# Performance work log

Measured on AMD Instinct MI355X. Metric: run time of the kernel, lower is better.

The kernel has to match this reference:

```python
import jax, jax.numpy as jnp
import numpy as np

N = 2048   # nodes in the tree
K = 2      # max children (heap-ordered binary tree)
IN = 1024  # in_dim
M = 1024   # mem_dim
L = 1024   # rows of the fixed attention matrix


def setup_inputs() -> dict:
    key = jax.random.key(0)
    ks = jax.random.split(key, 12)
    s_in = 1.0 / np.sqrt(IN)
    s_m = 1.0 / np.sqrt(M)
    inputs = jax.random.normal(ks[0], (N, IN), jnp.float32)
    hiddn_state_mat = jax.random.normal(ks[1], (L, M), jnp.float32)
    # heap-ordered binary tree: children of i are 2i+1, 2i+2; -1 = no child.
    ch = np.full((N, K), -1, dtype=np.int64)
    for k in range(K):
        c = 2 * np.arange(N) + 1 + k
        ch[:, k] = np.where(c < N, c, -1)
    children = jnp.asarray(ch)
    u = lambda k, shape, s: jax.random.uniform(k, shape, jnp.float32, -s, s)
    params = dict(
        ioux_w=u(ks[2], (3 * M, IN), s_in), ioux_b=u(ks[3], (3 * M,), s_in),
        iouh_w=u(ks[4], (3 * M, M), s_m),  iouh_b=u(ks[5], (3 * M,), s_m),
        fx_w=u(ks[6], (M, IN), s_in),      fx_b=u(ks[7], (M,), s_in),
        fh_w=u(ks[8], (M, M), s_m),        fh_b=u(ks[9], (M,), s_m),
        Wa=-0.05 + 0.05 * jax.random.normal(ks[10], (1, M), jnp.float32),
        attnh_w=u(ks[11], (M, 2 * M), s_m),
        attnh_b=jnp.zeros((M,), jnp.float32),
    )
    return dict(inputs=inputs, hiddn_state_mat=hiddn_state_mat, children=children, **params)


def reference(inputs, hiddn_state_mat, children, ioux_w, ioux_b, iouh_w, iouh_b,
              fx_w, fx_b, fh_w, fh_b, Wa, attnh_w, attnh_b):
    mask = (children >= 0)
    safe = jnp.where(mask, children, 0)
    # split attnh into the part acting on h (first M cols) and on hiddn_state_mat
    W1 = attnh_w[:, :M]  # [M, M]
    W2 = attnh_w[:, M:]  # [M, M]
    HW2 = hiddn_state_mat @ W2.T  # [L, M], constant across nodes
    x_iou = inputs @ ioux_w.T + ioux_b  # [N, 3M]
    x_f = inputs @ fx_w.T + fx_b        # [N, M]

    def step(carry, t):
        C, Hs = carry  # [N, M] each
        m = mask[t].astype(inputs.dtype)[:, None]        # [K, 1]
        c_ch = C[safe[t]] * m                            # [K, M] (zeros for pads == torch leaf zeros)
        h_ch = Hs[safe[t]] * m                           # [K, M]
        h_sum = h_ch.sum(0)                              # [M]
        iou = x_iou[t] + h_sum @ iouh_w.T + iouh_b       # [3M]
        i, o, u = jnp.split(iou, 3)
        i, o, u = jax.nn.sigmoid(i), jax.nn.sigmoid(o), jnp.tanh(u)
        f = jax.nn.sigmoid(h_ch @ fh_w.T + fh_b + x_f[t])  # [K, M]
        c = i * u + (f * c_ch).sum(0)                    # [M]
        h = o * jnp.tanh(c)                              # [M]
        # attention over the fixed hidden-state matrix
        a = jnp.tanh(h @ W1.T + HW2 + attnh_b)           # [L, M]
        p = jax.nn.softmax(a @ Wa[0])                    # [L]
        # sum(p[:,None]*h_tiled, 0) == sum(p)*h since rows are identical
        h = ((1.0 - p)[:, None] * hiddn_state_mat).sum(0) + jnp.sum(p) * h
        return (C.at[t].set(c), Hs.at[t].set(h)), None

    C0 = jnp.zeros((N, M), inputs.dtype)
    Hs0 = jnp.zeros((N, M), inputs.dtype)
    order = jnp.arange(N - 1, -1, -1)  # leaves first, root (node 0) last
    (C, Hs), _ = jax.lax.scan(step, (C0, Hs0), order)
    return C[0:1], Hs[0:1], Hs  # (root c, root h, all hidden states)
```

## Files before the change

kernel.cpp:

```cpp
#include <hip/hip_runtime.h>
#include <hip/hip_bf16.h>

#define MD 1024
#define LD 1024
#define ND 2048
#define JZ 4096

typedef __bf16 bf16x8 __attribute__((ext_vector_type(8)));
typedef __bf16 bf16x4 __attribute__((ext_vector_type(4)));
typedef float  f32x4  __attribute__((ext_vector_type(4)));

__device__ __forceinline__ float fsig(float x)  { return 1.0f / (1.0f + __expf(-x)); }
__device__ __forceinline__ float ftanh_(float x){ float e = __expf(2.0f * x); return 1.0f - 2.0f / (e + 1.0f); }

__device__ __forceinline__ bf16x8 bzero8() {
    bf16x8 z;
    #pragma unroll
    for (int q = 0; q < 8; q++) z[q] = (__bf16)0.f;
    return z;
}

__global__ void cvt_rows_k(const float* __restrict__ src, int ld,
                           __bf16* __restrict__ dst, int K)
{
    int j = blockIdx.y;
    int k = blockIdx.x * 256 + threadIdx.x;
    dst[(size_t)j * K + k] = (__bf16)src[(size_t)j * ld + k];
}

__global__ void concat_bias_k(const float* __restrict__ a, const float* __restrict__ b,
                              float* __restrict__ dst)
{
    int i = blockIdx.x * 256 + threadIdx.x;
    dst[i] = (i < 3 * MD) ? a[i] : b[i - 3 * MD];
}

__global__ __launch_bounds__(256) void gemm_mfma(
    const __bf16* __restrict__ Ab, const float* __restrict__ Af, int amode, int lda,
    const __bf16* __restrict__ Wh,
    const float* __restrict__ bias,
    const float* __restrict__ X, int ldx, const float* __restrict__ add1,
    float* __restrict__ C, float* __restrict__ C2, __bf16* __restrict__ C3, int ldc,
    int I, int K, float scale, int epi)
{
    __shared__ __align__(16) __bf16 Ash[4][128][8];
    __shared__ __align__(16) __bf16 Bsh[4][128][8];
    const int tid = threadIdx.x;
    const int j0 = blockIdx.x * 128, i0 = blockIdx.y * 128;
    const int lane = tid & 63, wv = tid >> 6;
    const int wm = wv >> 1, wn = wv & 1;
    const int g = lane >> 4, fr = lane & 15;

    f32x4 acc[4][4];
    #pragma unroll
    for (int m = 0; m < 4; m++)
        #pragma unroll
        for (int n = 0; n < 4; n++)
            acc[m][n] = (f32x4){0.f, 0.f, 0.f, 0.f};

    const int srow = tid >> 1;
    const int kh   = (tid & 1) * 16;
    const int g0   = kh >> 3;
    const int arow = i0 + srow;
    const bool rowok = arow < I;
    const __bf16* Wrow = Wh + (size_t)(j0 + srow) * K + kh;
    const __bf16* Abr = Ab + (size_t)arow * lda + kh;
    const float*  Afr = Af + (size_t)arow * lda + kh;

    for (int kt = 0; kt < K; kt += 32) {
        bf16x8 a0, a1;
        if (amode == 0) {
            if (rowok) { a0 = *(const bf16x8*)(Abr + kt); a1 = *(const bf16x8*)(Abr + kt + 8); }
            else       { a0 = bzero8(); a1 = bzero8(); }
        } else {
            float f[16];
            if (rowok) {
                *(float4*)&f[0]  = *(const float4*)(Afr + kt);
                *(float4*)&f[4]  = *(const float4*)(Afr + kt + 4);
                *(float4*)&f[8]  = *(const float4*)(Afr + kt + 8);
                *(float4*)&f[12] = *(const float4*)(Afr + kt + 12);
            } else {
                #pragma unroll
                for (int q = 0; q < 16; q++) f[q] = 0.f;
            }
            #pragma unroll
            for (int q = 0; q < 8; q++) { a0[q] = (__bf16)f[q]; a1[q] = (__bf16)f[8 + q]; }
        }
        bf16x8 w0 = *(const bf16x8*)(Wrow + kt);
        bf16x8 w1 = *(const bf16x8*)(Wrow + kt + 8);
        __syncthreads();
        *(bf16x8*)&Ash[g0][srow][0]     = a0;
        *(bf16x8*)&Ash[g0 + 1][srow][0] = a1;
        *(bf16x8*)&Bsh[g0][srow][0]     = w0;
        *(bf16x8*)&Bsh[g0 + 1][srow][0] = w1;
        __syncthreads();

        bf16x8 ah[4], bh[4];
        #pragma unroll
        for (int m = 0; m < 4; m++) ah[m] = *(bf16x8*)&Ash[g][wm * 64 + m * 16 + fr][0];
        #pragma unroll
        for (int n = 0; n < 4; n++) bh[n] = *(bf16x8*)&Bsh[g][wn * 64 + n * 16 + fr][0];
        #pragma unroll
        for (int m = 0; m < 4; m++)
            #pragma unroll
            for (int n = 0; n < 4; n++)
                acc[m][n] = __builtin_amdgcn_mfma_f32_16x16x32_bf16(ah[m], bh[n], acc[m][n], 0, 0, 0);
    }

    #pragma unroll
    for (int m = 0; m < 4; m++) {
        int rbase = i0 + wm * 64 + m * 16 + g * 4;
        #pragma unroll
        for (int nn = 0; nn < 4; nn++) {
            int col = j0 + wn * 64 + nn * 16 + fr;
            float b = bias ? bias[col] : 0.f;
            #pragma unroll
            for (int j = 0; j < 4; j++) {
                int r = rbase + j;
                if (r >= I) continue;
                float a = acc[m][nn][j];
                if (epi == 2) {
                    float hc = X[(size_t)r * ldx + col];
                    C[(size_t)r * ldc + col]  = add1[col] - a + hc;
                    float d = hc - a;
                    C2[(size_t)r * ldc + col] = d;
                    C3[(size_t)r * ldc + col] = (__bf16)d;
                } else {
                    float v = (a + b) * scale;
                    if (X) v += X[(size_t)r * ldx + col];
                    if (epi == 1) v = __expf(fminf(fmaxf(v, -80.f), 80.f));
                    C[(size_t)r * ldc + col] = v;
                }
            }
        }
    }
}

__global__ __launch_bounds__(256) void gemm64_mfma(
    const __bf16* __restrict__ Ab, const float* __restrict__ Af, int amode, int lda,
    const __bf16* __restrict__ Wh,
    const float* __restrict__ bias,
    const float* __restrict__ X, int ldx, const float* __restrict__ add1,
    float* __restrict__ C, float* __restrict__ C2, __bf16* __restrict__ C3, int ldc,
    int I, int K, float scale, int epi)
{
    __shared__ __align__(16) __bf16 Ash[4][64][8];
    __shared__ __align__(16) __bf16 Bsh[4][64][8];
    const int tid = threadIdx.x;
    const int j0 = blockIdx.x * 64, i0 = blockIdx.y * 64;
    const int lane = tid & 63, wv = tid >> 6;
    const int wm = wv >> 1, wn = wv & 1;
    const int g = lane >> 4, fr = lane & 15;

    f32x4 acc[2][2];
    #pragma unroll
    for (int m = 0; m < 2; m++)
        #pragma unroll
        for (int n = 0; n < 2; n++)
            acc[m][n] = (f32x4){0.f, 0.f, 0.f, 0.f};

    const int srow = tid >> 2;
    const int kh   = (tid & 3) * 8;
    const int g0   = kh >> 3;
    const int arow = i0 + srow;
    const bool rowok = arow < I;
    const __bf16* Wrow = Wh + (size_t)(j0 + srow) * K + kh;
    const __bf16* Abr = Ab + (size_t)arow * lda + kh;
    const float*  Afr = Af + (size_t)arow * lda + kh;

    for (int kt = 0; kt < K; kt += 32) {
        bf16x8 a0;
        if (amode == 0) {
            a0 = rowok ? *(const bf16x8*)(Abr + kt) : bzero8();
        } else {
            float f[8];
            if (rowok) {
                *(float4*)&f[0] = *(const float4*)(Afr + kt);
                *(float4*)&f[4] = *(const float4*)(Afr + kt + 4);
            } else {
                #pragma unroll
                for (int q = 0; q < 8; q++) f[q] = 0.f;
            }
            #pragma unroll
            for (int q = 0; q < 8; q++) a0[q] = (__bf16)f[q];
        }
        bf16x8 w0 = *(const bf16x8*)(Wrow + kt);
        __syncthreads();
        *(bf16x8*)&Ash[g0][srow][0] = a0;
        *(bf16x8*)&Bsh[g0][srow][0] = w0;
        __syncthreads();

        bf16x8 ah[2], bh[2];
        #pragma unroll
        for (int m = 0; m < 2; m++) ah[m] = *(bf16x8*)&Ash[g][wm * 32 + m * 16 + fr][0];
        #pragma unroll
        for (int n = 0; n < 2; n++) bh[n] = *(bf16x8*)&Bsh[g][wn * 32 + n * 16 + fr][0];
        #pragma unroll
        for (int m = 0; m < 2; m++)
            #pragma unroll
            for (int n = 0; n < 2; n++)
                acc[m][n] = __builtin_amdgcn_mfma_f32_16x16x32_bf16(ah[m], bh[n], acc[m][n], 0, 0, 0);
    }

    #pragma unroll
    for (int m = 0; m < 2; m++) {
        int rbase = i0 + wm * 32 + m * 16 + g * 4;
        #pragma unroll
        for (int nn = 0; nn < 2; nn++) {
            int col = j0 + wn * 32 + nn * 16 + fr;
            float b = bias ? bias[col] : 0.f;
            #pragma unroll
            for (int j = 0; j < 4; j++) {
                int r = rbase + j;
                if (r >= I) continue;
                float a = acc[m][nn][j];
                if (epi == 2) {
                    float hc = X[(size_t)r * ldx + col];
                    C[(size_t)r * ldc + col]  = add1[col] - a + hc;
                    float d = hc - a;
                    C2[(size_t)r * ldc + col] = d;
                    C3[(size_t)r * ldc + col] = (__bf16)d;
                } else {
                    float v = (a + b) * scale;
                    if (X) v += X[(size_t)r * ldx + col];
                    if (epi == 1) v = __expf(fminf(fmaxf(v, -80.f), 80.f));
                    C[(size_t)r * ldc + col] = v;
                }
            }
        }
    }
}

template<int IMAX, bool WB>
__global__ __launch_bounds__(256) void gemv_nt(
    const float* __restrict__ Af, int lda, int I,
    const __bf16* __restrict__ Wb, const float* __restrict__ Wf, int ldw,
    const float* __restrict__ bias,
    const float* __restrict__ X, int ldx, const float* __restrict__ add1,
    float* __restrict__ C, float* __restrict__ C2, __bf16* __restrict__ C3, int ldc,
    int K, float scale, int epi)
{
    const int wv = threadIdx.x >> 6, lane = threadIdx.x & 63;
    const int j = blockIdx.x * 4 + wv;
    float acc[IMAX];
    #pragma unroll
    for (int i = 0; i < IMAX; i++) acc[i] = 0.0f;
    for (int k = lane * 4; k < K; k += 256) {
        float w0, w1, w2, w3;
        if (WB) {
            bf16x4 w4 = *(const bf16x4*)(Wb + (size_t)j * K + k);
            w0 = (float)w4[0]; w1 = (float)w4[1]; w2 = (float)w4[2]; w3 = (float)w4[3];
        } else {
            float4 w4 = *(const float4*)(Wf + (size_t)j * ldw + k);
            w0 = w4.x; w1 = w4.y; w2 = w4.z; w3 = w4.w;
        }
        #pragma unroll
        for (int i = 0; i < IMAX; i++) {
            if (i < I) {
                float4 a4 = *(const float4*)(Af + (size_t)i * lda + k);
                acc[i] += a4.x * w0 + a4.y * w1 + a4.z * w2 + a4.w * w3;
            }
        }
    }
    #pragma unroll
    for (int i = 0; i < IMAX; i++) {
        if (i < I) {
            float s = acc[i];
            #pragma unroll
            for (int off = 32; off >= 1; off >>= 1) s += __shfl_xor(s, off);
            if (lane == 0) {
                if (epi == 2) {
                    float hc = X[(size_t)i * ldx + j];
                    C[(size_t)i * ldc + j]  = add1[j] - s + hc;
                    float d = hc - s;
                    C2[(size_t)i * ldc + j] = d;
                    C3[(size_t)i * ldc + j] = (__bf16)d;
                } else {
                    float v = (s + (bias ? bias[j] : 0.f)) * scale;
                    if (X) v += X[(size_t)i * ldx + j];
                    if (epi == 1) v = __expf(fminf(fmaxf(v, -80.f), 80.f));
                    C[(size_t)i * ldc + j] = v;
                }
            }
        }
    }
}

template<int LTILE>
__global__ __launch_bounds__(512) void attn_s(
    int B, const float* __restrict__ Eh,
    const float* __restrict__ EH,
    const float* __restrict__ s_wa_sum,
    const float* __restrict__ Wa,
    float* __restrict__ S)
{
    __shared__ float s_e[8][MD];
    __shared__ float s_wa[MD];
    const int lt = blockIdx.x * LTILE;
    const int b0 = blockIdx.y * 8;
    const int nt = (B - b0 < 8) ? (B - b0) : 8;
    for (int idx = threadIdx.x; idx < MD; idx += 512) s_wa[idx] = Wa[idx];
    for (int i = 0; i < nt; i++)
        for (int idx = threadIdx.x; idx < MD; idx += 512)
            s_e[i][idx] = Eh[(size_t)(b0 + i) * MD + idx];
    __syncthreads();
    const int wv = threadIdx.x >> 6, lane = threadIdx.x & 63;
    const float swa = s_wa_sum[0];
    if (LTILE >= 16) {
        for (int l = lt + wv; l < lt + LTILE; l += 16) {
            float accA[8] = {}, accB[8] = {};
            const float* erA = EH + (size_t)l * MD;
            const float* erB = EH + (size_t)(l + 8) * MD;
            for (int mc = 0; mc < MD; mc += 256) {
                const int m = mc + lane * 4;
                float4 evA = *(const float4*)(erA + m);
                float4 evB = *(const float4*)(erB + m);
                float4 wa4 = *(const float4*)&s_wa[m];
                #pragma unroll
                for (int i = 0; i < 8; i++) {
                    if (i < nt) {
                        float4 se = *(const float4*)&s_e[i][m];
                        accA[i] = fmaf(wa4.x, __builtin_amdgcn_rcpf(fmaf(se.x, evA.x, 1.0f)), accA[i]);
                        accA[i] = fmaf(wa4.y, __builtin_amdgcn_rcpf(fmaf(se.y, evA.y, 1.0f)), accA[i]);
                        accA[i] = fmaf(wa4.z, __builtin_amdgcn_rcpf(fmaf(se.z, evA.z, 1.0f)), accA[i]);
                        accA[i] = fmaf(wa4.w, __builtin_amdgcn_rcpf(fmaf(se.w, evA.w, 1.0f)), accA[i]);
                        accB[i] = fmaf(wa4.x, __builtin_amdgcn_rcpf(fmaf(se.x, evB.x, 1.0f)), accB[i]);
                        accB[i] = fmaf(wa4.y, __builtin_amdgcn_rcpf(fmaf(se.y, evB.y, 1.0f)), accB[i]);
                        accB[i] = fmaf(wa4.z, __builtin_amdgcn_rcpf(fmaf(se.z, evB.z, 1.0f)), accB[i]);
                        accB[i] = fmaf(wa4.w, __builtin_amdgcn_rcpf(fmaf(se.w, evB.w, 1.0f)), accB[i]);
                    }
                }
            }
            #pragma unroll
            for (int i = 0; i < 8; i++) {
                if (i < nt) {
                    float vA = accA[i], vB = accB[i];
                    #pragma unroll
                    for (int off = 32; off >= 1; off >>= 1) {
                        vA += __shfl_xor(vA, off);
                        vB += __shfl_xor(vB, off);
                    }
                    if (lane == 0) {
                        S[(size_t)(b0 + i) * LD + l]     = swa - 2.0f * vA;
                        S[(size_t)(b0 + i) * LD + l + 8] = swa - 2.0f * vB;
                    }
                }
            }
        }
    } else {
        for (int l = lt + wv; l < lt + LTILE; l += 8) {
            float acc[8] = {};
            const float* er = EH + (size_t)l * MD;
            for (int mc = 0; mc < MD; mc += 256) {
                const int m = mc + lane * 4;
                float4 ev  = *(const float4*)(er + m);
                float4 wa4 = *(const float4*)&s_wa[m];
                #pragma unroll
                for (int i = 0; i < 8; i++) {
                    if (i < nt) {
                        float4 se = *(const float4*)&s_e[i][m];
                        acc[i] = fmaf(wa4.x, __builtin_amdgcn_rcpf(fmaf(se.x, ev.x, 1.0f)), acc[i]);
                        acc[i] = fmaf(wa4.y, __builtin_amdgcn_rcpf(fmaf(se.y, ev.y, 1.0f)), acc[i]);
                        acc[i] = fmaf(wa4.z, __builtin_amdgcn_rcpf(fmaf(se.z, ev.z, 1.0f)), acc[i]);
                        acc[i] = fmaf(wa4.w, __builtin_amdgcn_rcpf(fmaf(se.w, ev.w, 1.0f)), acc[i]);
                    }
                }
            }
            #pragma unroll
            for (int i = 0; i < 8; i++) {
                if (i < nt) {
                    float v = acc[i];
                    #pragma unroll
                    for (int off = 32; off >= 1; off >>= 1) v += __shfl_xor(v, off);
                    if (lane == 0) S[(size_t)(b0 + i) * LD + l] = swa - 2.0f * v;
                }
            }
        }
    }
}

__global__ __launch_bounds__(256) void softmax_rows(float* __restrict__ S, __bf16* __restrict__ Sb)
{
    float* row = S + (size_t)blockIdx.x * LD;
    __bf16* rb = Sb + (size_t)blockIdx.x * LD;
    const int tid = threadIdx.x;
    const int wv = tid >> 6, lane = tid & 63;
    float v0 = row[tid], v1 = row[tid + 256], v2 = row[tid + 512], v3 = row[tid + 768];
    float mx = fmaxf(fmaxf(v0, v1), fmaxf(v2, v3));
    #pragma unroll
    for (int off = 32; off >= 1; off >>= 1) mx = fmaxf(mx, __shfl_xor(mx, off));
    __shared__ float r1[4], r2[4];
    if (lane == 0) r1[wv] = mx;
    __syncthreads();
    mx = fmaxf(fmaxf(r1[0], r1[1]), fmaxf(r1[2], r1[3]));
    float e0 = __expf(v0 - mx), e1 = __expf(v1 - mx), e2 = __expf(v2 - mx), e3 = __expf(v3 - mx);
    float sm = e0 + e1 + e2 + e3;
    #pragma unroll
    for (int off = 32; off >= 1; off >>= 1) sm += __shfl_xor(sm, off);
    if (lane == 0) r2[wv] = sm;
    __syncthreads();
    sm = r2[0] + r2[1] + r2[2] + r2[3];
    float inv = 1.0f / sm;
    float p0 = e0 * inv, p1 = e1 * inv, p2 = e2 * inv, p3 = e3 * inv;
    row[tid] = p0; row[tid + 256] = p1; row[tid + 512] = p2; row[tid + 768] = p3;
    rb[tid] = (__bf16)p0; rb[tid + 256] = (__bf16)p1;
    rb[tid + 512] = (__bf16)p2; rb[tid + 768] = (__bf16)p3;
}

__global__ void cell_finish_k(const int* __restrict__ children, int t0,
    const float* __restrict__ Z, const float* __restrict__ HsumWz,
    const float* __restrict__ iouh_b, const float* __restrict__ fh_b,
    const float* __restrict__ x_all,
    float* __restrict__ Cmat, float* __restrict__ hcell)
{
    int b = blockIdx.y;
    int m = blockIdx.x * 256 + threadIdx.x;
    int t = t0 + b;
    int c0 = children[2 * t], c1 = children[2 * t + 1];
    float cnt = (float)((c0 >= 0) + (c1 >= 0));
    const float* z0 = (c0 >= 0) ? Z + (size_t)c0 * JZ : nullptr;
    const float* z1 = (c1 >= 0) ? Z + (size_t)c1 * JZ : nullptr;
    const float* xr = x_all + (size_t)t * JZ;

    float zi = 0.f, zo = 0.f, zu = 0.f;
    if (z0) { zi += z0[m]; zo += z0[MD + m]; zu += z0[2 * MD + m]; }
    if (z1) { zi += z1[m]; zo += z1[MD + m]; zu += z1[2 * MD + m]; }
    float iv = fsig (zi + cnt * HsumWz[m]          + iouh_b[m]          + xr[m]);
    float ov = fsig (zo + cnt * HsumWz[MD + m]     + iouh_b[MD + m]     + xr[MD + m]);
    float uv = ftanh_(zu + cnt * HsumWz[2 * MD + m] + iouh_b[2 * MD + m] + xr[2 * MD + m]);

    float xf  = xr[3 * MD + m];
    float hwf = HsumWz[3 * MD + m] + fh_b[m] + xf;
    float c = iv * uv;
    if (c0 >= 0) {
        float f0 = fsig(z0[3 * MD + m] + hwf);
        c += f0 * Cmat[(size_t)c0 * MD + m];
    }
    if (c1 >= 0) {
        float f1 = fsig(z1[3 * MD + m] + hwf);
        c += f1 * Cmat[(size_t)c1 * MD + m];
    }
    Cmat[(size_t)t * MD + m] = c;
    hcell[(size_t)b * MD + m] = ov * ftanh_(c);
}

__global__ void colsum_part_k(const float* __restrict__ H, float* __restrict__ part)
{
    int m = blockIdx.x * 256 + threadIdx.x;
    int lb = blockIdx.y;
    float s = 0.f;
    for (int l = lb * 64; l < lb * 64 + 64; l++) s += H[(size_t)l * MD + m];
    part[(size_t)lb * MD + m] = s;
}

__global__ void colsum_reduce_k(const float* __restrict__ part, float* __restrict__ Hsum)
{
    int m = blockIdx.x * 256 + threadIdx.x;
    float s = 0.f;
    for (int lb = 0; lb < 16; lb++) s += part[(size_t)lb * MD + m];
    Hsum[m] = s;
}

__global__ void transpose2_k(const float* __restrict__ H,
                             float* __restrict__ Ht, __bf16* __restrict__ Htb)
{
    __shared__ float tile[32][33];
    int mb = blockIdx.x * 32, lb = blockIdx.y * 32;
    int tx = threadIdx.x, ty = threadIdx.y;
    #pragma unroll
    for (int jj = 0; jj < 4; jj++)
        tile[ty + jj * 8][tx] = H[(size_t)(lb + ty + jj * 8) * MD + mb + tx];
    __syncthreads();
    #pragma unroll
    for (int jj = 0; jj < 4; jj++) {
        float v = tile[tx][ty + jj * 8];
        size_t idx = (size_t)(mb + ty + jj * 8) * LD + lb + tx;
        Ht[idx]  = v;
        Htb[idx] = (__bf16)v;
    }
}

__global__ void sumwa_k(const float* __restrict__ Wa, float* __restrict__ out)
{
    int tid = threadIdx.x;
    float v = Wa[tid] + Wa[tid + 256] + Wa[tid + 512] + Wa[tid + 768];
    #pragma unroll
    for (int off = 32; off >= 1; off >>= 1) v += __shfl_xor(v, off);
    __shared__ float r[4];
    if ((tid & 63) == 0) r[tid >> 6] = v;
    __syncthreads();
    if (tid == 0) out[0] = r[0] + r[1] + r[2] + r[3];
}

__global__ void final_copy_k(const float* __restrict__ Cmat, float* __restrict__ out)
{
    int m = blockIdx.x * 256 + threadIdx.x;
    out[m] = Cmat[m];
    out[1024 + m] = out[2048 + m];
}

static inline void mmx(int amode,
                       const __bf16* Ab, const float* Af, int lda, int I,
                       const __bf16* Wb,
                       const float* bias, const float* X, int ldx, const float* add1,
                       float* C, float* C2, __bf16* C3, int ldc, int J, int K,
                       float scale, int epi, hipStream_t s)
{
    if (I <= 32) {
        gemv_nt<32, true><<<J / 4, 256, 0, s>>>(Af, lda, I, Wb, nullptr, K,
            bias, X, ldx, add1, C, C2, C3, ldc, K, scale, epi);
    } else {
        int b128 = (J / 128) * ((I + 127) / 128);
        if (b128 >= 192)
            gemm_mfma<<<dim3(J / 128, (I + 127) / 128), 256, 0, s>>>(
                Ab, Af, amode, lda, Wb, bias, X, ldx, add1, C, C2, C3, ldc, I, K, scale, epi);
        else
            gemm64_mfma<<<dim3(J / 64, (I + 63) / 64), 256, 0, s>>>(
                Ab, Af, amode, lda, Wb, bias, X, ldx, add1, C, C2, C3, ldc, I, K, scale, epi);
    }
}

extern "C" void kernel_launch(void* const* d_in, const int* in_sizes, int n_in,
                              void* d_out, int out_size, void* d_ws, size_t ws_size,
                              hipStream_t stream)
{
    const float* inputs   = (const float*)d_in[0];
    const float* Hmat     = (const float*)d_in[1];
    const int*   children = (const int*)d_in[2];
    const float* ioux_w   = (const float*)d_in[3];
    const float* ioux_b   = (const float*)d_in[4];
    const float* iouh_w   = (const float*)d_in[5];
    const float* iouh_b   = (const float*)d_in[6];
    const float* fx_w     = (const float*)d_in[7];
    const float* fx_b     = (const float*)d_in[8];
    const float* fh_w     = (const float*)d_in[9];
    const float* fh_b     = (const float*)d_in[10];
    const float* Wa       = (const float*)d_in[11];
    const float* attnh_w  = (const float*)d_in[12];
    const float* attnh_b  = (const float*)d_in[13];

    float* out = (float*)d_out;
    float* Hs  = out + 2048;

    float* p = (float*)d_ws;
    float* x_all   = p;  p += (size_t)ND * JZ;
    float* Zbuf    = p;  p += (size_t)ND * JZ;
    float* EHbuf   = p;  p += (size_t)LD * MD;
    float* Ht      = p;  p += (size_t)MD * LD;
    float* Cmat    = p;  p += (size_t)ND * MD;
    float* Hdelta  = p;  p += (size_t)ND * MD;
    float* hcell   = p;  p += (size_t)1024 * MD;
    float* Ehbuf   = p;  p += (size_t)1024 * MD;
    float* Sbuf    = p;  p += (size_t)1024 * LD;
    float* Hsum    = p;  p += MD;
    float* part16  = p;  p += 16 * MD;
    float* S_wa    = p;  p += 8;
    float* HsumWz  = p;  p += JZ;
    float* bx      = p;  p += JZ;
    __bf16* q = (__bf16*)p;
    __bf16* WzB    = q; q += (size_t)JZ * MD;
    __bf16* WxB    = q; q += (size_t)JZ * MD;
    __bf16* W1H    = q; q += (size_t)MD * MD;
    __bf16* W2H    = q; q += (size_t)MD * MD;
    __bf16* HtH    = q; q += (size_t)MD * LD;
    __bf16* inpB   = q; q += (size_t)ND * MD;
    __bf16* HmatB  = q; q += (size_t)LD * MD;
    __bf16* SbB    = q; q += (size_t)1024 * LD;
    __bf16* HdB    = q; q += (size_t)ND * MD;

    cvt_rows_k<<<dim3(4, 3 * MD), 256, 0, stream>>>(iouh_w, MD, WzB, MD);
    cvt_rows_k<<<dim3(4, MD), 256, 0, stream>>>(fh_w, MD, WzB + (size_t)3 * MD * MD, MD);
    cvt_rows_k<<<dim3(4, 3 * MD), 256, 0, stream>>>(ioux_w, MD, WxB, MD);
    cvt_rows_k<<<dim3(4, MD), 256, 0, stream>>>(fx_w, MD, WxB + (size_t)3 * MD * MD, MD);
    cvt_rows_k<<<dim3(4, MD), 256, 0, stream>>>(attnh_w, 2 * MD, W1H, MD);
    cvt_rows_k<<<dim3(4, MD), 256, 0, stream>>>(attnh_w + MD, 2 * MD, W2H, MD);
    cvt_rows_k<<<dim3(4, ND), 256, 0, stream>>>(inputs, MD, inpB, MD);
    cvt_rows_k<<<dim3(4, LD), 256, 0, stream>>>(Hmat, MD, HmatB, MD);
    concat_bias_k<<<JZ / 256, 256, 0, stream>>>(ioux_b, fx_b, bx);
    transpose2_k<<<dim3(32, 32), dim3(32, 8), 0, stream>>>(Hmat, Ht, HtH);
    sumwa_k<<<1, 256, 0, stream>>>(Wa, S_wa);
    colsum_part_k<<<dim3(4, 16), 256, 0, stream>>>(Hmat, part16);
    colsum_reduce_k<<<4, 256, 0, stream>>>(part16, Hsum);
    gemv_nt<1, false><<<(3 * MD) / 4, 256, 0, stream>>>(Hsum, MD, 1, nullptr, iouh_w, MD,
        nullptr, nullptr, 0, nullptr, HsumWz, nullptr, nullptr, 3 * MD, MD, 1.0f, 0);
    gemv_nt<1, false><<<MD / 4, 256, 0, stream>>>(Hsum, MD, 1, nullptr, fh_w, MD,
        nullptr, nullptr, 0, nullptr, HsumWz + 3 * MD, nullptr, nullptr, MD, MD, 1.0f, 0);

    mmx(0, inpB, nullptr, MD, ND, WxB, bx, nullptr, 0, nullptr,
        x_all, nullptr, nullptr, JZ, JZ, MD, 1.0f, 0, stream);
    mmx(0, HmatB, nullptr, MD, LD, W2H, attnh_b, nullptr, 0, nullptr,
        EHbuf, nullptr, nullptr, MD, MD, MD, 2.0f, 1, stream);

    static const int lv_t0[12] = {2047, 1023, 511, 255, 127, 63, 31, 15, 7, 3, 1, 0};
    static const int lv_B [12] = {1, 1024, 512, 256, 128, 64, 32, 16, 8, 4, 2, 1};
    for (int li = 0; li < 12; li++) {
        int t0 = lv_t0[li], B = lv_B[li];
        cell_finish_k<<<dim3(4, B), 256, 0, stream>>>(children, t0, Zbuf, HsumWz,
                                                      iouh_b, fh_b, x_all, Cmat, hcell);
        mmx(1, nullptr, hcell, MD, B, W1H, nullptr, nullptr, 0, nullptr,
            Ehbuf, nullptr, nullptr, MD, MD, MD, 2.0f, 1, stream);
        if (B >= 128)
            attn_s<64><<<dim3(LD / 64, B / 8), 512, 0, stream>>>(B, Ehbuf, EHbuf, S_wa, Wa, Sbuf);
        else
            attn_s<8><<<dim3(LD / 8, (B + 7) / 8), 512, 0, stream>>>(B, Ehbuf, EHbuf, S_wa, Wa, Sbuf);
        softmax_rows<<<B, 256, 0, stream>>>(Sbuf, SbB);
        mmx(0, SbB, Sbuf, LD, B, HtH, nullptr, hcell, MD, Hsum,
            Hs + (size_t)t0 * MD, Hdelta + (size_t)t0 * MD, HdB + (size_t)t0 * MD,
            MD, MD, LD, 1.0f, 2, stream);
        if (li < 11)
            mmx(0, HdB + (size_t)t0 * MD, Hdelta + (size_t)t0 * MD, MD, B, WzB,
                nullptr, nullptr, 0, nullptr,
                Zbuf + (size_t)t0 * JZ, nullptr, nullptr, JZ, JZ, MD, 1.0f, 0, stream);
    }
    final_copy_k<<<4, 256, 0, stream>>>(Cmat, out);
}
```

Measured before the change: 1.279 ms.

## Use direct global-to-LDS loads in MFMA GEMMs and emit bf16 hidden states

The MFMA GEMM tiles now load A and W straight into shared memory with global_load_lds, replacing register staging. The shared tile layout becomes row-major per k-group, and out-of-range rows are clamped to the last valid row instead of zero-filled. The fp32-to-bf16 A path is removed: cell_finish writes a bf16 copy of hcell, so the W1 GEMM reads bf16 directly. This aims to cut register traffic and conversion work in the GEMM inner loop, but adds an extra bf16 store. Clamped rows load duplicate data whose outputs are masked in the epilogue.

```diff
diff --git a/kernel.cpp b/kernel.cpp
--- a/kernel.cpp
+++ b/kernel.cpp
@@ -13,11 +13,11 @@
 __device__ __forceinline__ float fsig(float x)  { return 1.0f / (1.0f + __expf(-x)); }
 __device__ __forceinline__ float ftanh_(float x){ float e = __expf(2.0f * x); return 1.0f - 2.0f / (e + 1.0f); }
 
-__device__ __forceinline__ bf16x8 bzero8() {
-    bf16x8 z;
-    #pragma unroll
-    for (int q = 0; q < 8; q++) z[q] = (__bf16)0.f;
-    return z;
+__device__ __forceinline__ void gload16(const __bf16* g, __bf16* l)
+{
+    __builtin_amdgcn_global_load_lds(
+        (const __attribute__((address_space(1))) void*)g,
+        (__attribute__((address_space(3))) void*)l, 16, 0, 0);
 }
 
 __global__ void cvt_rows_k(const float* __restrict__ src, int ld,
@@ -36,15 +36,15 @@
 }
 
 __global__ __launch_bounds__(256) void gemm_mfma(
-    const __bf16* __restrict__ Ab, const float* __restrict__ Af, int amode, int lda,
+    const __bf16* __restrict__ Ab, int lda,
     const __bf16* __restrict__ Wh,
     const float* __restrict__ bias,
     const float* __restrict__ X, int ldx, const float* __restrict__ add1,
     float* __restrict__ C, float* __restrict__ C2, __bf16* __restrict__ C3, int ldc,
     int I, int K, float scale, int epi)
 {
-    __shared__ __align__(16) __bf16 Ash[4][128][8];
-    __shared__ __align__(16) __bf16 Bsh[4][128][8];
+    __shared__ __align__(16) __bf16 Ash[128][4][8];
+    __shared__ __align__(16) __bf16 Bsh[128][4][8];
     const int tid = threadIdx.x;
     const int j0 = blockIdx.x * 128, i0 = blockIdx.y * 128;
     const int lane = tid & 63, wv = tid >> 6;
@@ -58,48 +58,32 @@
         for (int n = 0; n < 4; n++)
             acc[m][n] = (f32x4){0.f, 0.f, 0.f, 0.f};
 
-    const int srow = tid >> 1;
-    const int kh   = (tid & 1) * 16;
-    const int g0   = kh >> 3;
-    const int arow = i0 + srow;
-    const bool rowok = arow < I;
-    const __bf16* Wrow = Wh + (size_t)(j0 + srow) * K + kh;
-    const __bf16* Abr = Ab + (size_t)arow * lda + kh;
-    const float*  Afr = Af + (size_t)arow * lda + kh;
+    const int srow = tid >> 2;
+    const int sg   = tid & 3;
+    int ar0 = i0 + srow;       if (ar0 >= I) ar0 = I - 1;
+    int ar1 = i0 + srow + 64;  if (ar1 >= I) ar1 = I - 1;
+    const __bf16* agp0 = Ab + (size_t)ar0 * lda + sg * 8;
+    const __bf16* agp1 = Ab + (size_t)ar1 * lda + sg * 8;
+    const __bf16* wgp0 = Wh + (size_t)(j0 + srow) * K + sg * 8;
+    const __bf16* wgp1 = Wh + (size_t)(j0 + srow + 64) * K + sg * 8;
+    __bf16* aD0 = &Ash[wv * 16][0][0];
+    __bf16* aD1 = &Ash[64 + wv * 16][0][0];
+    __bf16* bD0 = &Bsh[wv * 16][0][0];
+    __bf16* bD1 = &Bsh[64 + wv * 16][0][0];
 
     for (int kt = 0; kt < K; kt += 32) {
-        bf16x8 a0, a1;
-        if (amode == 0) {
-            if (rowok) { a0 = *(const bf16x8*)(Abr + kt); a1 = *(const bf16x8*)(Abr + kt + 8); }
-            else       { a0 = bzero8(); a1 = bzero8(); }
-        } else {
-            float f[16];
-            if (rowok) {
-                *(float4*)&f[0]  = *(const float4*)(Afr + kt);
-                *(float4*)&f[4]  = *(const float4*)(Afr + kt + 4);
-                *(float4*)&f[8]  = *(const float4*)(Afr + kt + 8);
-                *(float4*)&f[12] = *(const float4*)(Afr + kt + 12);
-            } else {
-                #pragma unroll
-                for (int q = 0; q < 16; q++) f[q] = 0.f;
-            }
-            #pragma unroll
-            for (int q = 0; q < 8; q++) { a0[q] = (__bf16)f[q]; a1[q] = (__bf16)f[8 + q]; }
-        }
-        bf16x8 w0 = *(const bf16x8*)(Wrow + kt);
-        bf16x8 w1 = *(const bf16x8*)(Wrow + kt + 8);
         __syncthreads();
-        *(bf16x8*)&Ash[g0][srow][0]     = a0;
-        *(bf16x8*)&Ash[g0 + 1][srow][0] = a1;
-        *(bf16x8*)&Bsh[g0][srow][0]     = w0;
-        *(bf16x8*)&Bsh[g0 + 1][srow][0] = w1;
+        gload16(agp0 + kt, aD0);
+        gload16(agp1 + kt, aD1);
+        gload16(wgp0 + kt, bD0);
+        gload16(wgp1 + kt, bD1);
         __syncthreads();
 
         bf16x8 ah[4], bh[4];
         #pragma unroll
-        for (int m = 0; m < 4; m++) ah[m] = *(bf16x8*)&Ash[g][wm * 64 + m * 16 + fr][0];
-        #pragma unroll
-        for (int n = 0; n < 4; n++) bh[n] = *(bf16x8*)&Bsh[g][wn * 64 + n * 16 + fr][0];
+        for (int m = 0; m < 4; m++) ah[m] = *(bf16x8*)&Ash[wm * 64 + m * 16 + fr][g][0];
+        #pragma unroll
+        for (int n = 0; n < 4; n++) bh[n] = *(bf16x8*)&Bsh[wn * 64 + n * 16 + fr][g][0];
         #pragma unroll
         for (int m = 0; m < 4; m++)
             #pragma unroll
@@ -137,15 +121,15 @@
 }
 
 __global__ __launch_bounds__(256) void gemm64_mfma(
-    const __bf16* __restrict__ Ab, const float* __restrict__ Af, int amode, int lda,
+    const __bf16* __restrict__ Ab, int lda,
     const __bf16* __restrict__ Wh,
     const float* __restrict__ bias,
     const float* __restrict__ X, int ldx, const float* __restrict__ add1,
     float* __restrict__ C, float* __restrict__ C2, __bf16* __restrict__ C3, int ldc,
     int I, int K, float scale, int epi)
 {
-    __shared__ __align__(16) __bf16 Ash[4][64][8];
-    __shared__ __align__(16) __bf16 Bsh[4][64][8];
+    __shared__ __align__(16) __bf16 Ash[64][4][8];
+    __shared__ __align__(16) __bf16 Bsh[64][4][8];
     const int tid = threadIdx.x;
     const int j0 = blockIdx.x * 64, i0 = blockIdx.y * 64;
     const int lane = tid & 63, wv = tid >> 6;
@@ -160,41 +144,24 @@
             acc[m][n] = (f32x4){0.f, 0.f, 0.f, 0.f};
 
     const int srow = tid >> 2;
-    const int kh   = (tid & 3) * 8;
-    const int g0   = kh >> 3;
-    const int arow = i0 + srow;
-    const bool rowok = arow < I;
-    const __bf16* Wrow = Wh + (size_t)(j0 + srow) * K + kh;
-    const __bf16* Abr = Ab + (size_t)arow * lda + kh;
-    const float*  Afr = Af + (size_t)arow * lda + kh;
+    const int sg   = tid & 3;
+    int ar = i0 + srow;  if (ar >= I) ar = I - 1;
+    const __bf16* agp = Ab + (size_t)ar * lda + sg * 8;
+    const __bf16* wgp = Wh + (size_t)(j0 + srow) * K + sg * 8;
+    __bf16* aD = &Ash[wv * 16][0][0];
+    __bf16* bD = &Bsh[wv * 16][0][0];
 
     for (int kt = 0; kt < K; kt += 32) {
-        bf16x8 a0;
-        if (amode == 0) {
-            a0 = rowok ? *(const bf16x8*)(Abr + kt) : bzero8();
-        } else {
-            float f[8];
-            if (rowok) {
-                *(float4*)&f[0] = *(const float4*)(Afr + kt);
-                *(float4*)&f[4] = *(const float4*)(Afr + kt + 4);
-            } else {
-                #pragma unroll
-                for (int q = 0; q < 8; q++) f[q] = 0.f;
-            }
-            #pragma unroll
-            for (int q = 0; q < 8; q++) a0[q] = (__bf16)f[q];
-        }
-        bf16x8 w0 = *(const bf16x8*)(Wrow + kt);
         __syncthreads();
-        *(bf16x8*)&Ash[g0][srow][0] = a0;
-        *(bf16x8*)&Bsh[g0][srow][0] = w0;
+        gload16(agp + kt, aD);
+        gload16(wgp + kt, bD);
         __syncthreads();
 
         bf16x8 ah[2], bh[2];
         #pragma unroll
-        for (int m = 0; m < 2; m++) ah[m] = *(bf16x8*)&Ash[g][wm * 32 + m * 16 + fr][0];
-        #pragma unroll
-        for (int n = 0; n < 2; n++) bh[n] = *(bf16x8*)&Bsh[g][wn * 32 + n * 16 + fr][0];
+        for (int m = 0; m < 2; m++) ah[m] = *(bf16x8*)&Ash[wm * 32 + m * 16 + fr][g][0];
+        #pragma unroll
+        for (int n = 0; n < 2; n++) bh[n] = *(bf16x8*)&Bsh[wn * 32 + n * 16 + fr][g][0];
         #pragma unroll
         for (int m = 0; m < 2; m++)
             #pragma unroll
@@ -411,7 +378,7 @@
     const float* __restrict__ Z, const float* __restrict__ HsumWz,
     const float* __restrict__ iouh_b, const float* __restrict__ fh_b,
     const float* __restrict__ x_all,
-    float* __restrict__ Cmat, float* __restrict__ hcell)
+    float* __restrict__ Cmat, float* __restrict__ hcell, __bf16* __restrict__ hcellB)
 {
     int b = blockIdx.y;
     int m = blockIdx.x * 256 + threadIdx.x;
@@ -425,9 +392,9 @@
     float zi = 0.f, zo = 0.f, zu = 0.f;
     if (z0) { zi += z0[m]; zo += z0[MD + m]; zu += z0[2 * MD + m]; }
     if (z1) { zi += z1[m]; zo += z1[MD + m]; zu += z1[2 * MD + m]; }
-    float iv = fsig (zi + cnt * HsumWz[m]          + iouh_b[m]          + xr[m]);
-    float ov = fsig (zo + cnt * HsumWz[MD + m]     + iouh_b[MD + m]     + xr[MD + m]);
-    float uv = ftanh_(zu + cnt * HsumWz[2 * MD + m] + iouh_b[2 * MD + m] + xr[2 * MD + m]);
+    float iv = fsig (zi + cnt * HsumWz[m]           + iouh_b[m]           + xr[m]);
+    float ov = fsig (zo + cnt * HsumWz[MD + m]      + iouh_b[MD + m]      + xr[MD + m]);
+    float uv = ftanh_(zu + cnt * HsumWz[2 * MD + m] + iouh_b[2 * MD + m]  + xr[2 * MD + m]);
 
     float xf  = xr[3 * MD + m];
     float hwf = HsumWz[3 * MD + m] + fh_b[m] + xf;
@@ -441,7 +408,9 @@
         c += f1 * Cmat[(size_t)c1 * MD + m];
     }
     Cmat[(size_t)t * MD + m] = c;
-    hcell[(size_t)b * MD + m] = ov * ftanh_(c);
+    float h = ov * ftanh_(c);
+    hcell[(size_t)b * MD + m] = h;
+    hcellB[(size_t)b * MD + m] = (__bf16)h;
 }
 
 __global__ void colsum_part_k(const float* __restrict__ H, float* __restrict__ part)
@@ -499,8 +468,7 @@
     out[1024 + m] = out[2048 + m];
 }
 
-static inline void mmx(int amode,
-                       const __bf16* Ab, const float* Af, int lda, int I,
+static inline void mmx(const __bf16* Ab, const float* Af, int lda, int I,
                        const __bf16* Wb,
                        const float* bias, const float* X, int ldx, const float* add1,
                        float* C, float* C2, __bf16* C3, int ldc, int J, int K,
@@ -513,10 +481,10 @@
         int b128 = (J / 128) * ((I + 127) / 128);
         if (b128 >= 192)
             gemm_mfma<<<dim3(J / 128, (I + 127) / 128), 256, 0, s>>>(
-                Ab, Af, amode, lda, Wb, bias, X, ldx, add1, C, C2, C3, ldc, I, K, scale, epi);
+                Ab, lda, Wb, bias, X, ldx, add1, C, C2, C3, ldc, I, K, scale, epi);
         else
             gemm64_mfma<<<dim3(J / 64, (I + 63) / 64), 256, 0, s>>>(
-                Ab, Af, amode, lda, Wb, bias, X, ldx, add1, C, C2, C3, ldc, I, K, scale, epi);
+                Ab, lda, Wb, bias, X, ldx, add1, C, C2, C3, ldc, I, K, scale, epi);
     }
 }
 
@@ -567,6 +535,7 @@
     __bf16* HmatB  = q; q += (size_t)LD * MD;
     __bf16* SbB    = q; q += (size_t)1024 * LD;
     __bf16* HdB    = q; q += (size_t)ND * MD;
+    __bf16* hcellB = q; q += (size_t)1024 * MD;
 
     cvt_rows_k<<<dim3(4, 3 * MD), 256, 0, stream>>>(iouh_w, MD, WzB, MD);
     cvt_rows_k<<<dim3(4, MD), 256, 0, stream>>>(fh_w, MD, WzB + (size_t)3 * MD * MD, MD);
@@ -586,9 +555,9 @@
     gemv_nt<1, false><<<MD / 4, 256, 0, stream>>>(Hsum, MD, 1, nullptr, fh_w, MD,
         nullptr, nullptr, 0, nullptr, HsumWz + 3 * MD, nullptr, nullptr, MD, MD, 1.0f, 0);
 
-    mmx(0, inpB, nullptr, MD, ND, WxB, bx, nullptr, 0, nullptr,
+    mmx(inpB, nullptr, MD, ND, WxB, bx, nullptr, 0, nullptr,
         x_all, nullptr, nullptr, JZ, JZ, MD, 1.0f, 0, stream);
-    mmx(0, HmatB, nullptr, MD, LD, W2H, attnh_b, nullptr, 0, nullptr,
+    mmx(HmatB, nullptr, MD, LD, W2H, attnh_b, nullptr, 0, nullptr,
         EHbuf, nullptr, nullptr, MD, MD, MD, 2.0f, 1, stream);
 
     static const int lv_t0[12] = {2047, 1023, 511, 255, 127, 63, 31, 15, 7, 3, 1, 0};
@@ -596,19 +565,19 @@
     for (int li = 0; li < 12; li++) {
         int t0 = lv_t0[li], B = lv_B[li];
         cell_finish_k<<<dim3(4, B), 256, 0, stream>>>(children, t0, Zbuf, HsumWz,
-                                                      iouh_b, fh_b, x_all, Cmat, hcell);
-        mmx(1, nullptr, hcell, MD, B, W1H, nullptr, nullptr, 0, nullptr,
+                                                      iouh_b, fh_b, x_all, Cmat, hcell, hcellB);
+        mmx(hcellB, hcell, MD, B, W1H, nullptr, nullptr, 0, nullptr,
             Ehbuf, nullptr, nullptr, MD, MD, MD, 2.0f, 1, stream);
         if (B >= 128)
             attn_s<64><<<dim3(LD / 64, B / 8), 512, 0, stream>>>(B, Ehbuf, EHbuf, S_wa, Wa, Sbuf);
         else
             attn_s<8><<<dim3(LD / 8, (B + 7) / 8), 512, 0, stream>>>(B, Ehbuf, EHbuf, S_wa, Wa, Sbuf);
         softmax_rows<<<B, 256, 0, stream>>>(Sbuf, SbB);
-        mmx(0, SbB, Sbuf, LD, B, HtH, nullptr, hcell, MD, Hsum,
+        mmx(SbB, Sbuf, LD, B, HtH, nullptr, hcell, MD, Hsum,
             Hs + (size_t)t0 * MD, Hdelta + (size_t)t0 * MD, HdB + (size_t)t0 * MD,
             MD, MD, LD, 1.0f, 2, stream);
         if (li < 11)
-            mmx(0, HdB + (size_t)t0 * MD, Hdelta + (size_t)t0 * MD, MD, B, WzB,
+            mmx(HdB + (size_t)t0 * MD, Hdelta + (size_t)t0 * MD, MD, B, WzB,
                 nullptr, nullptr, 0, nullptr,
                 Zbuf + (size_t)t0 * JZ, nullptr, nullptr, JZ, JZ, MD, 1.0f, 0, stream);
     }
```

Result: faster. 1.227 ms (-4.0%).
